# Performance work log

Measured on AMD Instinct MI355X. Metric: run time of the kernel, lower is better.

Reference implementation:

```python
import jax, jax.numpy as jnp
import numpy as np

D_MODEL = 1024
NHEAD = 16
HEAD_DIM = D_MODEL // NHEAD


def setup_inputs() -> dict:
    key = jax.random.key(0)
    ks = jax.random.split(key, 11)
    B, T = 2, 2048
    s = 1.0 / np.sqrt(D_MODEL)
    return {
        "query": jax.random.normal(ks[0], (B, T, D_MODEL), jnp.float32),
        "key": jax.random.normal(ks[1], (B, T, D_MODEL), jnp.float32),
        "value": jax.random.normal(ks[2], (B, T, D_MODEL), jnp.float32),
        "Wq": jax.random.normal(ks[3], (D_MODEL, D_MODEL), jnp.float32) * s,
        "bq": jnp.zeros((D_MODEL,), jnp.float32),
        "Wk": jax.random.normal(ks[4], (D_MODEL, D_MODEL), jnp.float32) * s,
        "bk": jnp.zeros((D_MODEL,), jnp.float32),
        "Wv": jax.random.normal(ks[5], (D_MODEL, D_MODEL), jnp.float32) * s,
        "bv": jnp.zeros((D_MODEL,), jnp.float32),
        "Wo": jax.random.normal(ks[6], (D_MODEL, D_MODEL), jnp.float32) * s,
        "bo": jnp.zeros((D_MODEL,), jnp.float32),
    }


def reference(query, key, value, Wq, bq, Wk, bk, Wv, bv, Wo, bo):
    B, T, _ = query.shape
    scale = HEAD_DIM ** -0.5
    # Linear projections (torch Linear: x @ W.T + b)
    Q = query @ Wq.T + bq
    K = key @ Wk.T + bk
    V = value @ Wv.T + bv
    # [B, H, T, hd]
    Q = Q.reshape(B, T, NHEAD, HEAD_DIM).transpose(0, 2, 1, 3)
    K = K.reshape(B, T, NHEAD, HEAD_DIM).transpose(0, 2, 1, 3)
    V = V.reshape(B, T, NHEAD, HEAD_DIM).transpose(0, 2, 1, 3)
    # Attention scores [B, H, T, T]
    scores = jnp.einsum("bhqd,bhkd->bhqk", Q, K) * scale
    probs = jax.nn.softmax(scores, axis=-1)
    # dropout is identity in eval mode
    out = jnp.einsum("bhqk,bhkd->bhqd", probs, V)
    out = out.transpose(0, 2, 1, 3).reshape(B, T, D_MODEL)
    return out @ Wo.T + bo
```

## Files before the change

kernel.cpp:

```cpp
#include <hip/hip_runtime.h>
#include <stdint.h>

#define LOG2E_OVER_SQRTHD 0.18033688011112042f
#define SM_BIAS 12.0f

typedef unsigned short u16;
typedef _Float16 f16;
typedef __attribute__((ext_vector_type(4))) float f32x4;
typedef __attribute__((ext_vector_type(8))) _Float16 f16x8;

static __device__ __forceinline__ u16 f2h_bits(float f) {
  union { f16 h; u16 u; } v; v.h = (f16)f; return v.u;
}

static __device__ __forceinline__ void g2l16(const void* g, void* l) {
  __builtin_amdgcn_global_load_lds((const __attribute__((address_space(1))) void*)g,
                                   (__attribute__((address_space(3))) void*)l,
                                   16, 0, 0);
}

__global__ __launch_bounds__(256) void pack_all(
    const float* __restrict__ q, const float* __restrict__ k, const float* __restrict__ v,
    const float* __restrict__ wq, const float* __restrict__ wk,
    const float* __restrict__ wv, const float* __restrict__ wo,
    u16* __restrict__ X, u16* __restrict__ W) {
  int flat = blockIdx.x * 256 + threadIdx.x;
  const float* src;
  u16* dst;
  int idx;
  if (flat < 3 * 1048576) {
    int z = flat >> 20;
    idx = flat & 1048575;
    src = (z == 0) ? q : (z == 1) ? k : v;
    dst = X + (size_t)z * 4194304;
  } else {
    int f2 = flat - 3 * 1048576;
    int z = f2 >> 18;
    idx = f2 & 262143;
    src = (z == 0) ? wq : (z == 1) ? wk : (z == 2) ? wv : wo;
    dst = W + (size_t)z * 1048576;
  }
  float4 x = ((const float4*)src)[idx];
  ushort4 o;
  o.x = f2h_bits(x.x); o.y = f2h_bits(x.y); o.z = f2h_bits(x.z); o.w = f2h_bits(x.w);
  *(ushort4*)(dst + (size_t)idx * 4) = o;
}

template <bool OUT_F16>
static __device__ __forceinline__ void gemm_body(
    const u16* __restrict__ A, const u16* __restrict__ W,
    const float* __restrict__ bias, void* __restrict__ C,
    int ldc, bool row_bias, float oscale, int bm, int bn) {
  __shared__ u16 As[2][128 * 32];
  __shared__ u16 Bs[2][128 * 32];
  const int tid = threadIdx.x;
  const int lane = tid & 63;
  const int wave = tid >> 6;
  const int wm = wave >> 1, wn = wave & 1;
  const int quad = lane >> 4, l15 = lane & 15;

  f32x4 acc[4][4] = {};

  const int r0 = tid >> 2;
  const int c0 = (tid & 3) * 8;
  const u16* Ab = A + (size_t)bm * 1024 + (size_t)r0 * 1024 + c0;
  const u16* Wb = W + (size_t)bn * 1024 + (size_t)r0 * 1024 + c0;

  g2l16(Ab, As[0] + tid * 8);
  g2l16(Ab + 64 * 1024, As[0] + (256 + tid) * 8);
  g2l16(Wb, Bs[0] + tid * 8);
  g2l16(Wb + 64 * 1024, Bs[0] + (256 + tid) * 8);
  __syncthreads();

  for (int kt = 0; kt < 32; ++kt) {
    const int p = kt & 1;
    if (kt + 1 < 32) {
      const int kc = (kt + 1) * 32;
      g2l16(Ab + kc, As[p ^ 1] + tid * 8);
      g2l16(Ab + 64 * 1024 + kc, As[p ^ 1] + (256 + tid) * 8);
      g2l16(Wb + kc, Bs[p ^ 1] + tid * 8);
      g2l16(Wb + 64 * 1024 + kc, Bs[p ^ 1] + (256 + tid) * 8);
    }
    f16x8 af[4], bw[4];
#pragma unroll
    for (int mt = 0; mt < 4; ++mt)
      af[mt] = *(const f16x8*)(As[p] + (wm * 64 + mt * 16 + l15) * 32 + quad * 8);
#pragma unroll
    for (int nt = 0; nt < 4; ++nt)
      bw[nt] = *(const f16x8*)(Bs[p] + (wn * 64 + nt * 16 + l15) * 32 + quad * 8);
#pragma unroll
    for (int mt = 0; mt < 4; ++mt)
#pragma unroll
      for (int nt = 0; nt < 4; ++nt)
        acc[mt][nt] = __builtin_amdgcn_mfma_f32_16x16x32_f16(af[mt], bw[nt], acc[mt][nt], 0, 0, 0);
    __syncthreads();
  }

#pragma unroll
  for (int mt = 0; mt < 4; ++mt) {
    const int row = bm + wm * 64 + mt * 16 + quad * 4;
#pragma unroll
    for (int nt = 0; nt < 4; ++nt) {
      const int col = bn + wn * 64 + nt * 16 + l15;
      const float bcol = row_bias ? 0.0f : bias[col];
#pragma unroll
      for (int i = 0; i < 4; ++i) {
        const float bb = row_bias ? bias[row + i] : bcol;
        float val = (acc[mt][nt][i] + bb) * oscale;
        if (OUT_F16)
          ((u16*)C)[(size_t)(row + i) * ldc + col] = f2h_bits(val);
        else
          ((float*)C)[(size_t)(row + i) * ldc + col] = val;
      }
    }
  }
}

__global__ __launch_bounds__(256) void gemm_qkv(const u16* __restrict__ X,
    const u16* __restrict__ Wf, const float* __restrict__ bq,
    const float* __restrict__ bk, const float* __restrict__ bv,
    u16* __restrict__ QK, u16* __restrict__ Vt, float qscale) {
  const int z = blockIdx.z;
  if (z == 0) {
    gemm_body<true>(X, Wf, bq, QK, 1024, false, qscale,
                    blockIdx.x * 128, blockIdx.y * 128);
  } else if (z == 1) {
    gemm_body<true>(X + (size_t)4194304, Wf + (size_t)1048576, bk,
                    QK + (size_t)4194304, 1024, false, 1.0f,
                    blockIdx.x * 128, blockIdx.y * 128);
  } else {
    gemm_body<true>(Wf + (size_t)2 * 1048576, X + (size_t)2 * 4194304, bv,
                    Vt, 4096, true, 1.0f,
                    blockIdx.y * 128, blockIdx.x * 128);
  }
}

__global__ __launch_bounds__(256) void gemm_out(const u16* __restrict__ O,
    const u16* __restrict__ Wo, const float* __restrict__ bo,
    float* __restrict__ out) {
  gemm_body<false>(O, Wo, bo, out, 1024, false, 1.0f,
                   blockIdx.x * 128, blockIdx.y * 128);
}

__global__ __launch_bounds__(256) void attn_kernel(const u16* __restrict__ QK,
                                                   const u16* __restrict__ Vt,
                                                   u16* __restrict__ O) {
  constexpr int LSP = 68;
  __shared__ u16 Qs[64 * 64];
  __shared__ u16 Ks[64 * 64];
  __shared__ u16 Vts[64 * 64];
  __shared__ u16 Ps[4][16 * LSP];

  const u16* Qb = QK;
  const u16* Kb = QK + (size_t)4096 * 1024;

  const int tid = threadIdx.x, lane = tid & 63, wave = tid >> 6;
  const int quad = lane >> 4, l15 = lane & 15;

  const int id = blockIdx.x;
  const int xcd = id & 7;
  const int j = id >> 3;
  const int qt = j & 31;
  const int hb = xcd + 8 * (j >> 5);
  const int h = hb & 15, b = hb >> 4;

  const size_t qrow0 = (size_t)b * 2048 + qt * 64;
  const size_t kv0 = (size_t)b * 2048;
  const int hc = h * 64;

  const int r0 = tid >> 3;
  const int p0 = tid & 7;
  const int s0 = (p0 ^ (r0 & 7)) * 8;

  g2l16(Qb + (qrow0 + r0) * 1024 + hc + s0, Qs + tid * 8);
  g2l16(Qb + (qrow0 + 32 + r0) * 1024 + hc + s0, Qs + (256 + tid) * 8);
  __syncthreads();

  const int Rq = wave * 16 + l15;
  const f16x8 aq0 = *(const f16x8*)(Qs + Rq * 64 + ((quad ^ (Rq & 7)) * 8));
  const f16x8 aq1 = *(const f16x8*)(Qs + Rq * 64 + (((quad + 4) ^ (Rq & 7)) * 8));

  f32x4 o_acc[4] = {};
  float l_part[4] = {0.f, 0.f, 0.f, 0.f};
  u16* Pw = Ps[wave];

  for (int kt = 0; kt < 32; ++kt) {
    const size_t kr0 = kv0 + (size_t)kt * 64;
    __syncthreads();
    g2l16(Kb + (kr0 + r0) * 1024 + hc + s0, Ks + tid * 8);
    g2l16(Kb + (kr0 + 32 + r0) * 1024 + hc + s0, Ks + (256 + tid) * 8);
    g2l16(Vt + (size_t)(hc + r0) * 4096 + kr0 + s0, Vts + tid * 8);
    g2l16(Vt + (size_t)(hc + 32 + r0) * 4096 + kr0 + s0, Vts + (256 + tid) * 8);
    __syncthreads();

    f32x4 s[4];
#pragma unroll
    for (int nt = 0; nt < 4; ++nt)
      s[nt] = f32x4{-SM_BIAS, -SM_BIAS, -SM_BIAS, -SM_BIAS};
#pragma unroll
    for (int nt = 0; nt < 4; ++nt) {
      const int Rk = nt * 16 + l15;
      f16x8 bk0 = *(const f16x8*)(Ks + Rk * 64 + ((quad ^ (Rk & 7)) * 8));
      f16x8 bk1 = *(const f16x8*)(Ks + Rk * 64 + (((quad + 4) ^ (Rk & 7)) * 8));
      s[nt] = __builtin_amdgcn_mfma_f32_16x16x32_f16(aq0, bk0, s[nt], 0, 0, 0);
      s[nt] = __builtin_amdgcn_mfma_f32_16x16x32_f16(aq1, bk1, s[nt], 0, 0, 0);
    }

#pragma unroll
    for (int nt = 0; nt < 4; ++nt)
#pragma unroll
      for (int i = 0; i < 4; ++i) {
        float pe = __builtin_amdgcn_exp2f(s[nt][i]);
        l_part[i] += pe;
        Pw[(quad * 4 + i) * LSP + nt * 16 + l15] = f2h_bits(pe);
      }
    asm volatile("s_waitcnt lgkmcnt(0)" ::: "memory");

    union { f16x8 v; struct { uint2 lo, hi; } h; } ap0, ap1;
    ap0.h.lo = *(const uint2*)(Pw + l15 * LSP + quad * 8);
    ap0.h.hi = *(const uint2*)(Pw + l15 * LSP + quad * 8 + 4);
    ap1.h.lo = *(const uint2*)(Pw + l15 * LSP + 32 + quad * 8);
    ap1.h.hi = *(const uint2*)(Pw + l15 * LSP + 32 + quad * 8 + 4);
#pragma unroll
    for (int ct = 0; ct < 4; ++ct) {
      const int Rv = ct * 16 + l15;
      f16x8 bv0 = *(const f16x8*)(Vts + Rv * 64 + ((quad ^ (Rv & 7)) * 8));
      f16x8 bv1 = *(const f16x8*)(Vts + Rv * 64 + (((quad + 4) ^ (Rv & 7)) * 8));
      o_acc[ct] = __builtin_amdgcn_mfma_f32_16x16x32_f16(ap0.v, bv0, o_acc[ct], 0, 0, 0);
      o_acc[ct] = __builtin_amdgcn_mfma_f32_16x16x32_f16(ap1.v, bv1, o_acc[ct], 0, 0, 0);
    }
  }

#pragma unroll
  for (int i = 0; i < 4; ++i)
#pragma unroll
    for (int d = 1; d < 16; d <<= 1) l_part[i] += __shfl_xor(l_part[i], d);

#pragma unroll
  for (int i = 0; i < 4; ++i) {
    const float inv = 1.0f / l_part[i];
    const size_t row = qrow0 + wave * 16 + quad * 4 + i;
#pragma unroll
    for (int ct = 0; ct < 4; ++ct) {
      float ov = o_acc[ct][i] * inv;
      int col = hc + ct * 16 + l15;
      O[row * 1024 + col] = f2h_bits(ov);
    }
  }
}

extern "C" void kernel_launch(void* const* d_in, const int* in_sizes, int n_in,
                              void* d_out, int out_size, void* d_ws, size_t ws_size,
                              hipStream_t stream) {
  const float* query = (const float*)d_in[0];
  const float* key   = (const float*)d_in[1];
  const float* value = (const float*)d_in[2];
  const float* Wq = (const float*)d_in[3];
  const float* bq = (const float*)d_in[4];
  const float* Wk = (const float*)d_in[5];
  const float* bk = (const float*)d_in[6];
  const float* Wv = (const float*)d_in[7];
  const float* bv = (const float*)d_in[8];
  const float* Wo = (const float*)d_in[9];
  const float* bo = (const float*)d_in[10];
  float* out = (float*)d_out;

  u16* X  = (u16*)d_ws;
  u16* W  = X + (size_t)3 * 4194304;
  u16* QK = W + (size_t)4 * 1048576;
  u16* Vt = QK + (size_t)2 * 4194304;
  u16* O  = X;

  pack_all<<<dim3(16384, 1, 1), 256, 0, stream>>>(query, key, value, Wq, Wk, Wv, Wo, X, W);
  gemm_qkv<<<dim3(32, 8, 3), 256, 0, stream>>>(X, W, bq, bk, bv, QK, Vt,
                                               LOG2E_OVER_SQRTHD);
  attn_kernel<<<dim3(1024, 1, 1), 256, 0, stream>>>(QK, Vt, O);
  gemm_out<<<dim3(32, 8, 1), 256, 0, stream>>>(O, W + (size_t)3 * 1048576, bo, out);
}
```

Baseline: 243.0 us.

## Double attention query tile to 128 rows per block for K/V reuse

Each attention block now handles 128 query rows instead of 64, with every wave computing two 16-row M-tiles against the same K and V tiles in LDS. This halves the number of K/V tile loads and barriers per query row and gives each wave more MFMA work per shared-memory fetch. In exchange the grid shrinks from 1024 to 512 blocks and register and LDS use per block grow, which can lower occupancy and leave parts of the GPU underused.

Result: no change. 238.9 us (-1.7%).

```diff
diff --git a/kernel.cpp b/kernel.cpp
--- a/kernel.cpp
+++ b/kernel.cpp
@@ -146,10 +146,10 @@
                                                    const u16* __restrict__ Vt,
                                                    u16* __restrict__ O) {
   constexpr int LSP = 68;
-  __shared__ u16 Qs[64 * 64];
+  __shared__ u16 Qs[128 * 64];
   __shared__ u16 Ks[64 * 64];
   __shared__ u16 Vts[64 * 64];
-  __shared__ u16 Ps[4][16 * LSP];
+  __shared__ u16 Ps[4][32 * LSP];
 
   const u16* Qb = QK;
   const u16* Kb = QK + (size_t)4096 * 1024;
@@ -160,11 +160,11 @@
   const int id = blockIdx.x;
   const int xcd = id & 7;
   const int j = id >> 3;
-  const int qt = j & 31;
-  const int hb = xcd + 8 * (j >> 5);
+  const int qt = j & 15;
+  const int hb = xcd + 8 * (j >> 4);
   const int h = hb & 15, b = hb >> 4;
 
-  const size_t qrow0 = (size_t)b * 2048 + qt * 64;
+  const size_t qrow0 = (size_t)b * 2048 + qt * 128;
   const size_t kv0 = (size_t)b * 2048;
   const int hc = h * 64;
 
@@ -174,14 +174,20 @@
 
   g2l16(Qb + (qrow0 + r0) * 1024 + hc + s0, Qs + tid * 8);
   g2l16(Qb + (qrow0 + 32 + r0) * 1024 + hc + s0, Qs + (256 + tid) * 8);
+  g2l16(Qb + (qrow0 + 64 + r0) * 1024 + hc + s0, Qs + (512 + tid) * 8);
+  g2l16(Qb + (qrow0 + 96 + r0) * 1024 + hc + s0, Qs + (768 + tid) * 8);
   __syncthreads();
 
-  const int Rq = wave * 16 + l15;
-  const f16x8 aq0 = *(const f16x8*)(Qs + Rq * 64 + ((quad ^ (Rq & 7)) * 8));
-  const f16x8 aq1 = *(const f16x8*)(Qs + Rq * 64 + (((quad + 4) ^ (Rq & 7)) * 8));
-
-  f32x4 o_acc[4] = {};
-  float l_part[4] = {0.f, 0.f, 0.f, 0.f};
+  f16x8 aq[2][2];
+#pragma unroll
+  for (int mt = 0; mt < 2; ++mt) {
+    const int Rq = wave * 32 + mt * 16 + l15;
+    aq[mt][0] = *(const f16x8*)(Qs + Rq * 64 + ((quad ^ (Rq & 7)) * 8));
+    aq[mt][1] = *(const f16x8*)(Qs + Rq * 64 + (((quad + 4) ^ (Rq & 7)) * 8));
+  }
+
+  f32x4 o_acc[2][4] = {};
+  float l_part[2][4] = {};
   u16* Pw = Ps[wave];
 
   for (int kt = 0; kt < 32; ++kt) {
@@ -193,60 +199,78 @@
     g2l16(Vt + (size_t)(hc + 32 + r0) * 4096 + kr0 + s0, Vts + (256 + tid) * 8);
     __syncthreads();
 
-    f32x4 s[4];
-#pragma unroll
-    for (int nt = 0; nt < 4; ++nt)
-      s[nt] = f32x4{-SM_BIAS, -SM_BIAS, -SM_BIAS, -SM_BIAS};
+    f32x4 s[2][4];
+#pragma unroll
+    for (int mt = 0; mt < 2; ++mt)
+#pragma unroll
+      for (int nt = 0; nt < 4; ++nt)
+        s[mt][nt] = f32x4{-SM_BIAS, -SM_BIAS, -SM_BIAS, -SM_BIAS};
 #pragma unroll
     for (int nt = 0; nt < 4; ++nt) {
       const int Rk = nt * 16 + l15;
       f16x8 bk0 = *(const f16x8*)(Ks + Rk * 64 + ((quad ^ (Rk & 7)) * 8));
       f16x8 bk1 = *(const f16x8*)(Ks + Rk * 64 + (((quad + 4) ^ (Rk & 7)) * 8));
-      s[nt] = __builtin_amdgcn_mfma_f32_16x16x32_f16(aq0, bk0, s[nt], 0, 0, 0);
-      s[nt] = __builtin_amdgcn_mfma_f32_16x16x32_f16(aq1, bk1, s[nt], 0, 0, 0);
-    }
-
-#pragma unroll
-    for (int nt = 0; nt < 4; ++nt)
-#pragma unroll
-      for (int i = 0; i < 4; ++i) {
-        float pe = __builtin_amdgcn_exp2f(s[nt][i]);
-        l_part[i] += pe;
-        Pw[(quad * 4 + i) * LSP + nt * 16 + l15] = f2h_bits(pe);
+#pragma unroll
+      for (int mt = 0; mt < 2; ++mt) {
+        s[mt][nt] = __builtin_amdgcn_mfma_f32_16x16x32_f16(aq[mt][0], bk0, s[mt][nt], 0, 0, 0);
+        s[mt][nt] = __builtin_amdgcn_mfma_f32_16x16x32_f16(aq[mt][1], bk1, s[mt][nt], 0, 0, 0);
       }
+    }
+
+#pragma unroll
+    for (int mt = 0; mt < 2; ++mt)
+#pragma unroll
+      for (int nt = 0; nt < 4; ++nt)
+#pragma unroll
+        for (int i = 0; i < 4; ++i) {
+          float pe = __builtin_amdgcn_exp2f(s[mt][nt][i]);
+          l_part[mt][i] += pe;
+          Pw[(mt * 16 + quad * 4 + i) * LSP + nt * 16 + l15] = f2h_bits(pe);
+        }
     asm volatile("s_waitcnt lgkmcnt(0)" ::: "memory");
 
-    union { f16x8 v; struct { uint2 lo, hi; } h; } ap0, ap1;
-    ap0.h.lo = *(const uint2*)(Pw + l15 * LSP + quad * 8);
-    ap0.h.hi = *(const uint2*)(Pw + l15 * LSP + quad * 8 + 4);
-    ap1.h.lo = *(const uint2*)(Pw + l15 * LSP + 32 + quad * 8);
-    ap1.h.hi = *(const uint2*)(Pw + l15 * LSP + 32 + quad * 8 + 4);
+    union U { f16x8 v; struct { uint2 lo, hi; } h; } ap0[2], ap1[2];
+#pragma unroll
+    for (int mt = 0; mt < 2; ++mt) {
+      const u16* Pr = Pw + (mt * 16 + l15) * LSP;
+      ap0[mt].h.lo = *(const uint2*)(Pr + quad * 8);
+      ap0[mt].h.hi = *(const uint2*)(Pr + quad * 8 + 4);
+      ap1[mt].h.lo = *(const uint2*)(Pr + 32 + quad * 8);
+      ap1[mt].h.hi = *(const uint2*)(Pr + 32 + quad * 8 + 4);
+    }
 #pragma unroll
     for (int ct = 0; ct < 4; ++ct) {
       const int Rv = ct * 16 + l15;
       f16x8 bv0 = *(const f16x8*)(Vts + Rv * 64 + ((quad ^ (Rv & 7)) * 8));
       f16x8 bv1 = *(const f16x8*)(Vts + Rv * 64 + (((quad + 4) ^ (Rv & 7)) * 8));
-      o_acc[ct] = __builtin_amdgcn_mfma_f32_16x16x32_f16(ap0.v, bv0, o_acc[ct], 0, 0, 0);
-      o_acc[ct] = __builtin_amdgcn_mfma_f32_16x16x32_f16(ap1.v, bv1, o_acc[ct], 0, 0, 0);
-    }
-  }
-
-#pragma unroll
-  for (int i = 0; i < 4; ++i)
-#pragma unroll
-    for (int d = 1; d < 16; d <<= 1) l_part[i] += __shfl_xor(l_part[i], d);
-
-#pragma unroll
-  for (int i = 0; i < 4; ++i) {
-    const float inv = 1.0f / l_part[i];
-    const size_t row = qrow0 + wave * 16 + quad * 4 + i;
-#pragma unroll
-    for (int ct = 0; ct < 4; ++ct) {
-      float ov = o_acc[ct][i] * inv;
-      int col = hc + ct * 16 + l15;
-      O[row * 1024 + col] = f2h_bits(ov);
-    }
-  }
+#pragma unroll
+      for (int mt = 0; mt < 2; ++mt) {
+        o_acc[mt][ct] = __builtin_amdgcn_mfma_f32_16x16x32_f16(ap0[mt].v, bv0, o_acc[mt][ct], 0, 0, 0);
+        o_acc[mt][ct] = __builtin_amdgcn_mfma_f32_16x16x32_f16(ap1[mt].v, bv1, o_acc[mt][ct], 0, 0, 0);
+      }
+    }
+  }
+
+#pragma unroll
+  for (int mt = 0; mt < 2; ++mt)
+#pragma unroll
+    for (int i = 0; i < 4; ++i)
+#pragma unroll
+      for (int d = 1; d < 16; d <<= 1) l_part[mt][i] += __shfl_xor(l_part[mt][i], d);
+
+#pragma unroll
+  for (int mt = 0; mt < 2; ++mt)
+#pragma unroll
+    for (int i = 0; i < 4; ++i) {
+      const float inv = 1.0f / l_part[mt][i];
+      const size_t row = qrow0 + wave * 32 + mt * 16 + quad * 4 + i;
+#pragma unroll
+      for (int ct = 0; ct < 4; ++ct) {
+        float ov = o_acc[mt][ct][i] * inv;
+        int col = hc + ct * 16 + l15;
+        O[row * 1024 + col] = f2h_bits(ov);
+      }
+    }
 }
 
 extern "C" void kernel_launch(void* const* d_in, const int* in_sizes, int n_in,
@@ -274,6 +298,6 @@
   pack_all<<<dim3(16384, 1, 1), 256, 0, stream>>>(query, key, value, Wq, Wk, Wv, Wo, X, W);
   gemm_qkv<<<dim3(32, 8, 3), 256, 0, stream>>>(X, W, bq, bk, bv, QK, Vt,
                                                LOG2E_OVER_SQRTHD);
-  attn_kernel<<<dim3(1024, 1, 1), 256, 0, stream>>>(QK, Vt, O);
+  attn_kernel<<<dim3(512, 1, 1), 256, 0, stream>>>(QK, Vt, O);
   gemm_out<<<dim3(32, 8, 1), 256, 0, stream>>>(O, W + (size_t)3 * 1048576, bo, out);
 }
```
